# Kernel tuning notes

Measured on AMD Instinct MI355X. Metric: run time of the kernel, lower is better.

The kernel has to match this reference:

```python
import jax, jax.numpy as jnp
import numpy as np
from jax import lax

B, S, V, E, H = 64, 512, 50000, 300, 256


def _run_lstm(x, w_ih, w_hh, b_ih, b_hh, reverse):
    # x: [B,S,D]; w_ih: [4H,D]; w_hh: [4H,H]. PyTorch gate order: i,f,g,o.
    gx = jnp.einsum('bsd,gd->sbg', x, w_ih) + b_ih + b_hh  # [S,B,4H]
    Hh = w_hh.shape[1]

    def step(carry, g):
        h, c = carry
        g = g + h @ w_hh.T
        i, f, gg, o = jnp.split(g, 4, axis=-1)
        c = jax.nn.sigmoid(f) * c + jax.nn.sigmoid(i) * jnp.tanh(gg)
        h = jax.nn.sigmoid(o) * jnp.tanh(c)
        return (h, c), h

    init = (jnp.zeros((x.shape[0], Hh), x.dtype), jnp.zeros((x.shape[0], Hh), x.dtype))
    _, hs = lax.scan(step, init, gx, reverse=reverse)  # outputs aligned to input time order
    return jnp.swapaxes(hs, 0, 1)  # [B,S,H]


def _bilstm(x, wif, whf, bif, bhf, wib, whb, bib, bhb):
    fwd = _run_lstm(x, wif, whf, bif, bhf, False)
    bwd = _run_lstm(x, wib, whb, bib, bhb, True)
    return jnp.concatenate([fwd, bwd], axis=-1)  # [B,S,2H]


def setup_inputs() -> dict:
    key = jax.random.key(0)
    ks = iter(jax.random.split(key, 32))
    k = 1.0 / np.sqrt(H)
    u = lambda shape: jax.random.uniform(next(ks), shape, jnp.float32, -k, k)
    inp = {
        'input_ids': jax.random.randint(next(ks), (B, S), 0, V),
        'labels': jax.random.uniform(next(ks), (B, S), jnp.float32),
        'input_masks': jnp.ones((B, S), jnp.int64),
        'emb': jax.random.normal(next(ks), (V, E), jnp.float32) * 0.1,
    }
    # layer 0 (input E), layer 1 (input 2H); forward and backward directions
    for layer, d_in in ((0, E), (1, 2 * H)):
        for direc in ('f', 'b'):
            inp[f'w_ih_l{layer}{direc}'] = u((4 * H, d_in))
            inp[f'w_hh_l{layer}{direc}'] = u((4 * H, H))
            inp[f'b_ih_l{layer}{direc}'] = u((4 * H,))
            inp[f'b_hh_l{layer}{direc}'] = u((4 * H,))
    inp['w_lin'] = u((H,))
    inp['b_lin'] = u(())
    return inp


def reference(input_ids, labels, input_masks, emb,
              w_ih_l0f, w_hh_l0f, b_ih_l0f, b_hh_l0f,
              w_ih_l0b, w_hh_l0b, b_ih_l0b, b_hh_l0b,
              w_ih_l1f, w_hh_l1f, b_ih_l1f, b_hh_l1f,
              w_ih_l1b, w_hh_l1b, b_ih_l1b, b_hh_l1b,
              w_lin, b_lin):
    x = emb[input_ids]  # one-shot gather, replaces the double python loop: [B,S,E]
    h1 = _bilstm(x, w_ih_l0f, w_hh_l0f, b_ih_l0f, b_hh_l0f,
                 w_ih_l0b, w_hh_l0b, b_ih_l0b, b_hh_l0b)
    h2 = _bilstm(h1, w_ih_l1f, w_hh_l1f, b_ih_l1f, b_hh_l1f,
                 w_ih_l1b, w_hh_l1b, b_ih_l1b, b_hh_l1b)  # [B,S,2H]
    b, s = h2.shape[0], h2.shape[1]
    mean_dir = h2.reshape(b, s, 2, H).mean(axis=2)  # mean over directions
    scores = jax.nn.sigmoid(jnp.einsum('bsh,h->bs', mean_dir, w_lin) + b_lin)
    mask = input_masks.astype(scores.dtype)
    err = (scores - labels) ** 2 * mask
    loss = jnp.mean(jnp.sum(err, axis=1) / jnp.sum(mask, axis=1))
    return scores, loss
```

## Files before the change

### kernel.cpp

```cpp
#include <hip/hip_runtime.h>
#include <hip/hip_bf16.h>
#include <stdint.h>

#define B_  64
#define S_  512
#define E_  300
#define H_  256
#define T_  (B_*S_)
#define G4H 1024

using half8  = __attribute__((ext_vector_type(8))) _Float16;
using half4  = __attribute__((ext_vector_type(4))) _Float16;
using float4v = __attribute__((ext_vector_type(4))) float;

union H2 { _Float16 h[2]; uint32_t u; };

__device__ inline float sigm(float x) { return 1.f / (1.f + __expf(-x)); }
__device__ inline float tanhf_(float x) {
  float cx = fminf(fmaxf(x, -15.f), 15.f);
  float e = __expf(2.f * cx);
  return (e - 1.f) / (e + 1.f);
}

#define BARRIER() asm volatile("s_waitcnt lgkmcnt(0)\n\ts_barrier" ::: "memory")

__device__ inline void ld3_sc0(const uint64_t* p0, const uint64_t* p1,
                               const uint64_t* p2, uint4& a, uint4& b, uint4& c) {
  asm volatile(
      "global_load_dwordx4 %0, %3, off sc0\n\t"
      "global_load_dwordx4 %1, %4, off sc0\n\t"
      "global_load_dwordx4 %2, %5, off sc0\n\t"
      "s_waitcnt vmcnt(0)"
      : "=&v"(a), "=&v"(b), "=&v"(c)
      : "v"(p0), "v"(p1), "v"(p2) : "memory");
}
__device__ inline void st_sc0(uint64_t* p, uint64_t v) {
  asm volatile("global_store_dwordx2 %0, %1, off sc0" :: "v"(p), "v"(v) : "memory");
}
__device__ inline uint4 ldx4_pin(const _Float16* p) {
  uint4 r;
  asm volatile("global_load_dwordx4 %0, %1, off\n\ts_waitcnt vmcnt(0)"
               : "=v"(r) : "v"(p));
  return r;
}
__device__ inline int xcc_id() {
  int x;
  asm volatile("s_getreg_b32 %0, hwreg(HW_REG_XCC_ID, 0, 32)" : "=s"(x));
  return x & 7;
}

__global__ __launch_bounds__(256) void k_prep_wih(const float* __restrict__ wf,
    const float* __restrict__ wb, _Float16* __restrict__ Bt,
    int KIN, int KP, int total)
{
  int idx = blockIdx.x * 256 + threadIdx.x;
  if (idx >= total) return;
  int n = idx / KP, k = idx % KP;
  int dd = n >> 10, nn = n & 1023;
  int row = (nn & 3) * 256 + (nn >> 2);
  const float* src = dd ? wb : wf;
  Bt[idx] = (_Float16)(k < KIN ? src[row * KIN + k] : 0.f);
}

__global__ __launch_bounds__(256) void k_prep_whh(const float* __restrict__ wf,
    const float* __restrict__ wb, _Float16* __restrict__ Wr)
{
  int idx = blockIdx.x * 256 + threadIdx.x;
  int dd = idx >> 18;
  int rem = idx & 262143;
  int n = rem >> 8, k = rem & 255;
  int row = (n & 3) * 256 + (n >> 2);
  Wr[idx] = (_Float16)((dd ? wb : wf)[row * 256 + k]);
}

__global__ void k_prep_bias(const float* __restrict__ bif, const float* __restrict__ bhf,
    const float* __restrict__ bib, const float* __restrict__ bhb, float* __restrict__ bias)
{
  int n = blockIdx.x * 256 + threadIdx.x;
  int dd = n >> 10, nn = n & 1023;
  int row = (nn & 3) * 256 + (nn >> 2);
  bias[n] = dd ? (bib[row] + bhb[row]) : (bif[row] + bhf[row]);
}

__global__ __launch_bounds__(256) void k_gather(const int* __restrict__ ids,
    const float* __restrict__ emb, _Float16* __restrict__ xbf)
{
  int idx = blockIdx.x * 256 + threadIdx.x;
  int tt = idx / 40;
  int ch = idx % 40;
  int b = tt & 63, s = tt >> 6;
  int id = ids[b * S_ + s];
  const float* src = emb + (size_t)id * E_ + ch * 8;
  half8 v;
#pragma unroll
  for (int e = 0; e < 8; ++e) {
    int k = ch * 8 + e;
    v[e] = (_Float16)(k < E_ ? src[e] : 0.f);
  }
  *(half8*)(xbf + (size_t)tt * 320 + ch * 8) = v;
}

template<int K>
__global__ __launch_bounds__(256) void k_gemm(const _Float16* __restrict__ A,
    const _Float16* __restrict__ Bt, const float* __restrict__ bias,
    _Float16* __restrict__ gx)
{
  __shared__ _Float16 sA[128 * 72];
  __shared__ _Float16 sB[128 * 72];
  const int tid = threadIdx.x;
  const int t0 = blockIdx.y * 128;
  const int n0 = blockIdx.x * 128;
  const int lane = tid & 63, wid = tid >> 6;
  const int l15 = lane & 15, q = lane >> 4;
  const int wm = wid & 1, wn = wid >> 1;

  float4v acc[4][4] = {};

  for (int kt = 0; kt < K / 64; ++kt) {
    __syncthreads();
#pragma unroll
    for (int c = 0; c < 4; ++c) {
      int f = tid * 4 + c;
      int row = f >> 3, seg = f & 7;
      *(half8*)&sA[row * 72 + seg * 8] =
          *(const half8*)(A + (size_t)(t0 + row) * K + kt * 64 + seg * 8);
      *(half8*)&sB[row * 72 + seg * 8] =
          *(const half8*)(Bt + (size_t)(n0 + row) * K + kt * 64 + seg * 8);
    }
    __syncthreads();
#pragma unroll
    for (int kk = 0; kk < 2; ++kk) {
      half8 a[4], b[4];
#pragma unroll
      for (int mt = 0; mt < 4; ++mt)
        a[mt] = *(const half8*)&sA[(wm * 64 + mt * 16 + l15) * 72 + kk * 32 + q * 8];
#pragma unroll
      for (int nt = 0; nt < 4; ++nt)
        b[nt] = *(const half8*)&sB[(wn * 64 + nt * 16 + l15) * 72 + kk * 32 + q * 8];
#pragma unroll
      for (int mt = 0; mt < 4; ++mt)
#pragma unroll
        for (int nt = 0; nt < 4; ++nt)
          acc[mt][nt] = __builtin_amdgcn_mfma_f32_16x16x32_f16(a[mt], b[nt], acc[mt][nt], 0, 0, 0);
    }
  }

#pragma unroll
  for (int mt = 0; mt < 4; ++mt) {
#pragma unroll
    for (int nt = 0; nt < 4; ++nt) {
      int token = t0 + wm * 64 + mt * 16 + q * 4;
      int n = n0 + wn * 64 + nt * 16 + l15;
      float bs = bias[n];
      size_t base = (size_t)(n >> 10) * ((size_t)T_ * G4H) + (size_t)token * G4H + (n & 1023);
#pragma unroll
      for (int r = 0; r < 4; ++r)
        gx[base + (size_t)r * G4H] = (_Float16)(acc[mt][nt][r] + bs);
    }
  }
}

template<int LAYER>
__global__ __launch_bounds__(256, 1) void k_rec(const _Float16* __restrict__ gx,
    const _Float16* __restrict__ Wr, uint64_t* __restrict__ hxf,
    uint64_t* __restrict__ hxs, _Float16* __restrict__ h1bf,
    float* __restrict__ pd2, const float* __restrict__ w_lin,
    int* __restrict__ claim)
{
  const int tid = threadIdx.x;
  __shared__ int role_sh;

  if (tid == 0) {
    int xcd = xcc_id();
    int slot = __hip_atomic_fetch_add(claim + xcd, 1, __ATOMIC_RELAXED,
                                      __HIP_MEMORY_SCOPE_AGENT);
    int role = -1;
    if (slot < 4) {
      role = xcd * 4 + slot;
    } else {
      for (int it = 0;; ++it) {
        int s = 0, deficit = -1;
        for (int x = 0; x < 8; ++x) {
          int v = __hip_atomic_load(claim + x, __ATOMIC_RELAXED,
                                    __HIP_MEMORY_SCOPE_AGENT);
          s += (v < 4 ? v : 4);
          if (v < 4) deficit = x;
        }
        if (s == 32) break;
        if (it > 8 && deficit >= 0) {
          int r = __hip_atomic_fetch_add(claim + deficit, 1, __ATOMIC_RELAXED,
                                         __HIP_MEMORY_SCOPE_AGENT);
          if (r < 4) { role = deficit * 4 + r; break; }
        }
        __builtin_amdgcn_s_sleep(64);
      }
    }
    role_sh = role;
  }
  __syncthreads();
  const int role = role_sh;
  if (role < 0) return;

  const int cg = role >> 2, rg = role & 3;
  const int d = cg >> 2, g = cg & 3;
  const int lane = tid & 63, wv = tid >> 6;
  const int l15 = lane & 15, q = lane >> 4;
  const int b0g = g * 16;
  const int n0g = rg * 256;

  __shared__ _Float16 hstage[16 * 288];
  __shared__ float    preS[16 * 260];

  for (int i = tid; i < 16 * 144; i += 256)
    ((uint32_t*)hstage)[i] = 0u;

  uint4 wreg[4][8];
#pragma unroll
  for (int nt = 0; nt < 4; ++nt)
#pragma unroll
    for (int kt = 0; kt < 8; ++kt)
      wreg[nt][kt] = ldx4_pin(Wr +
          (size_t)(d * G4H + n0g + wv * 64 + nt * 16 + l15) * H_ + kt * 32 + q * 8);

  const int bl = tid >> 4;
  const int jl4 = (tid & 15) * 4;
  const int bglob = b0g + bl;
  const int jg = rg * 64 + jl4;
  float wl[4];
#pragma unroll
  for (int cc = 0; cc < 4; ++cc) wl[cc] = w_lin[jg + cc];
  float creg[4] = {0.f, 0.f, 0.f, 0.f};

  uint64_t* fbase = hxf + (size_t)cg * 2 * 2048;
  uint64_t* sbase = hxs + (size_t)cg * 2 * 2048;
  const int off2 = tid * 2;
  const int q2a = (rg + 1) & 3, q2b = (rg + 2) & 3, q2c = (rg + 3) & 3;

  half8 gxa, gxb;
  {
    const int time0 = d ? (S_ - 1) : 0;
    const _Float16* gp = gx + ((size_t)d * T_ + (size_t)time0 * B_ + bglob) * G4H
                           + n0g + (tid & 15) * 16;
    gxa = *(const half8*)(gp);
    gxb = *(const half8*)(gp + 8);
  }

  for (int t = 0; t < S_; ++t) {
    const int time = d ? (S_ - 1 - t) : t;

    if (t > 0) {
      const uint64_t* fs = fbase + (size_t)(t & 1) * 2048;
      const uint64_t* ss = sbase + (size_t)(t & 1) * 2048;
      const uint32_t tt = (uint32_t)t;
      uint32_t dat[6];
      unsigned pend = 0x3fu;
      int round = 0;
      while (pend) {
        uint4 A, Bv, C;
        ld3_sc0(fs + q2a * 512 + off2, fs + q2b * 512 + off2,
                fs + q2c * 512 + off2, A, Bv, C);
        if ((pend & 1u)  && A.y  == tt) { dat[0] = A.x;  pend &= ~1u; }
        if ((pend & 2u)  && A.w  == tt) { dat[1] = A.z;  pend &= ~2u; }
        if ((pend & 4u)  && Bv.y == tt) { dat[2] = Bv.x; pend &= ~4u; }
        if ((pend & 8u)  && Bv.w == tt) { dat[3] = Bv.z; pend &= ~8u; }
        if ((pend & 16u) && C.y  == tt) { dat[4] = C.x;  pend &= ~16u; }
        if ((pend & 32u) && C.w  == tt) { dat[5] = C.z;  pend &= ~32u; }
        if (pend && ((++round & 3) == 0)) {
          const int wq[3] = {q2a, q2b, q2c};
#pragma unroll
          for (int k3 = 0; k3 < 3; ++k3)
#pragma unroll
            for (int j = 0; j < 2; ++j) {
              int w = k3 * 2 + j;
              if (pend & (1u << w)) {
                uint64_t v = __hip_atomic_load(ss + wq[k3] * 512 + off2 + j,
                                               __ATOMIC_RELAXED, __HIP_MEMORY_SCOPE_AGENT);
                if ((uint32_t)(v >> 32) == tt) { dat[w] = (uint32_t)v; pend &= ~(1u << w); }
              }
            }
        }
      }
      const int sb = tid >> 4, jp = (tid & 15) * 2;
      uint2 va; va.x = dat[0]; va.y = dat[1];
      uint2 vb; vb.x = dat[2]; vb.y = dat[3];
      uint2 vc; vc.x = dat[4]; vc.y = dat[5];
      *(uint2*)&((uint32_t*)hstage)[sb * 144 + q2a * 32 + jp] = va;
      *(uint2*)&((uint32_t*)hstage)[sb * 144 + q2b * 32 + jp] = vb;
      *(uint2*)&((uint32_t*)hstage)[sb * 144 + q2c * 32 + jp] = vc;
    }
    BARRIER();

    half8 gxa_n, gxb_n;
    {
      const int tn = (t + 1 < S_) ? t + 1 : t;
      const int timen = d ? (S_ - 1 - tn) : tn;
      const _Float16* gp = gx + ((size_t)d * T_ + (size_t)timen * B_ + bglob) * G4H
                             + n0g + (tid & 15) * 16;
      gxa_n = *(const half8*)(gp);
      gxb_n = *(const half8*)(gp + 8);
    }

    float4v acc[4] = {};
#pragma unroll
    for (int kt = 0; kt < 8; ++kt) {
      half8 a = *(const half8*)&hstage[l15 * 288 + kt * 32 + q * 8];
#pragma unroll
      for (int nt = 0; nt < 4; ++nt)
        acc[nt] = __builtin_amdgcn_mfma_f32_16x16x32_f16(
            a, __builtin_bit_cast(half8, wreg[nt][kt]), acc[nt], 0, 0, 0);
    }
#pragma unroll
    for (int nt = 0; nt < 4; ++nt)
#pragma unroll
      for (int r = 0; r < 4; ++r)
        preS[(q * 4 + r) * 260 + wv * 64 + nt * 16 + l15] = acc[nt][r];
    BARRIER();

    half4 hv4;
    float partial = 0.f;
#pragma unroll
    for (int cc = 0; cc < 4; ++cc) {
      float4v p = *(const float4v*)&preS[bl * 260 + (jl4 + cc) * 4];
      float gxi = (float)(cc < 2 ? gxa[cc * 4 + 0] : gxb[(cc - 2) * 4 + 0]);
      float gxf = (float)(cc < 2 ? gxa[cc * 4 + 1] : gxb[(cc - 2) * 4 + 1]);
      float gxg = (float)(cc < 2 ? gxa[cc * 4 + 2] : gxb[(cc - 2) * 4 + 2]);
      float gxo = (float)(cc < 2 ? gxa[cc * 4 + 3] : gxb[(cc - 2) * 4 + 3]);
      float gi = p[0] + gxi, gf = p[1] + gxf, gg = p[2] + gxg, go = p[3] + gxo;
      float cv = sigm(gf) * creg[cc] + sigm(gi) * tanhf_(gg);
      float hv = sigm(go) * tanhf_(cv);
      creg[cc] = cv;
      hv4[cc] = (_Float16)hv;
      if (LAYER == 1) partial += 0.5f * hv * wl[cc];
    }

    {
      H2 p0; p0.h[0] = hv4[0]; p0.h[1] = hv4[1];
      H2 p1; p1.h[0] = hv4[2]; p1.h[1] = hv4[3];
      uint32_t tg = (uint32_t)(t + 1);
      uint64_t w0 = ((uint64_t)tg << 32) | p0.u;
      uint64_t w1 = ((uint64_t)tg << 32) | p1.u;
      uint64_t* fd = fbase + (size_t)((t + 1) & 1) * 2048 + rg * 512 + off2;
      st_sc0(fd + 0, w0);
      st_sc0(fd + 1, w1);
      uint64_t* sd = sbase + (size_t)((t + 1) & 1) * 2048 + rg * 512 + off2;
      __hip_atomic_store(sd + 0, w0, __ATOMIC_RELAXED, __HIP_MEMORY_SCOPE_AGENT);
      __hip_atomic_store(sd + 1, w1, __ATOMIC_RELAXED, __HIP_MEMORY_SCOPE_AGENT);
    }

    *(half4*)&hstage[bl * 288 + jg] = hv4;

    if (LAYER == 0) {
      *(half4*)(h1bf + ((size_t)time * B_ + bglob) * 512 + d * H_ + jg) = hv4;
    } else {
      partial += __shfl_xor(partial, 1);
      partial += __shfl_xor(partial, 2);
      partial += __shfl_xor(partial, 4);
      partial += __shfl_xor(partial, 8);
      if ((tid & 15) == 0)
        atomicAdd(pd2 + ((size_t)d * B_ + bglob) * S_ + time, partial);
    }

    gxa = gxa_n; gxb = gxb_n;
  }
}

__global__ __launch_bounds__(256) void k_final(const float* __restrict__ pd2,
    const float* __restrict__ labels, const int* __restrict__ masks,
    const float* __restrict__ b_lin, float* __restrict__ out)
{
  int b = blockIdx.x;
  int tid = threadIdx.x;
  float bl = b_lin[0];
  float se = 0.f, sm = 0.f;
  for (int s = tid; s < S_; s += 256) {
    float p = pd2[(size_t)b * S_ + s] + pd2[(size_t)(B_ + b) * S_ + s];
    float sc = sigm(p + bl);
    out[b * S_ + s] = sc;
    float m = (float)masks[b * S_ + s];
    float e = sc - labels[b * S_ + s];
    se += e * e * m;
    sm += m;
  }
  for (int off = 1; off < 64; off <<= 1) {
    se += __shfl_xor(se, off);
    sm += __shfl_xor(sm, off);
  }
  __shared__ float rs[4], rm[4];
  int wid = tid >> 6;
  if ((tid & 63) == 0) { rs[wid] = se; rm[wid] = sm; }
  __syncthreads();
  if (tid == 0) {
    float te = 0.f, tm = 0.f;
    for (int w = 0; w < 4; ++w) { te += rs[w]; tm += rm[w]; }
    atomicAdd(out + T_, (te / tm) * (1.f / 64.f));
  }
}

extern "C" void kernel_launch(void* const* d_in, const int* in_sizes, int n_in,
                              void* d_out, int out_size, void* d_ws, size_t ws_size,
                              hipStream_t stream)
{
  (void)in_sizes; (void)n_in; (void)out_size; (void)ws_size;
  const int*   ids    = (const int*)d_in[0];
  const float* labels = (const float*)d_in[1];
  const int*   masks  = (const int*)d_in[2];
  const float* emb    = (const float*)d_in[3];
  const float* w_ih_0f = (const float*)d_in[4];
  const float* w_hh_0f = (const float*)d_in[5];
  const float* b_ih_0f = (const float*)d_in[6];
  const float* b_hh_0f = (const float*)d_in[7];
  const float* w_ih_0b = (const float*)d_in[8];
  const float* w_hh_0b = (const float*)d_in[9];
  const float* b_ih_0b = (const float*)d_in[10];
  const float* b_hh_0b = (const float*)d_in[11];
  const float* w_ih_1f = (const float*)d_in[12];
  const float* w_hh_1f = (const float*)d_in[13];
  const float* b_ih_1f = (const float*)d_in[14];
  const float* b_hh_1f = (const float*)d_in[15];
  const float* w_ih_1b = (const float*)d_in[16];
  const float* w_hh_1b = (const float*)d_in[17];
  const float* b_ih_1b = (const float*)d_in[18];
  const float* b_hh_1b = (const float*)d_in[19];
  const float* w_lin   = (const float*)d_in[20];
  const float* b_lin   = (const float*)d_in[21];
  float* out = (float*)d_out;

  char* ws = (char*)d_ws;
  size_t off = 0;
  auto alloc = [&](size_t bytes) -> char* {
    char* p = ws + off;
    off += (bytes + 255) & ~(size_t)255;
    return p;
  };
  _Float16* xbf   = (_Float16*)alloc((size_t)T_ * 320 * 2);
  _Float16* h1bf  = (_Float16*)alloc((size_t)T_ * 512 * 2);
  _Float16* gx    = (_Float16*)alloc((size_t)2 * T_ * G4H * 2);
  _Float16* Bt0   = (_Float16*)alloc((size_t)2048 * 320 * 2);
  _Float16* Bt1   = (_Float16*)alloc((size_t)2048 * 512 * 2);
  _Float16* Wr0   = (_Float16*)alloc((size_t)2 * G4H * H_ * 2);
  _Float16* Wr1   = (_Float16*)alloc((size_t)2 * G4H * H_ * 2);
  float*    bias0 = (float*)alloc(2048 * 4);
  float*    bias1 = (float*)alloc(2048 * 4);
  uint64_t* hxf0  = (uint64_t*)alloc((size_t)8 * 2 * 2048 * 8);
  uint64_t* hxs0  = (uint64_t*)alloc((size_t)8 * 2 * 2048 * 8);
  uint64_t* hxf1  = (uint64_t*)alloc((size_t)8 * 2 * 2048 * 8);
  uint64_t* hxs1  = (uint64_t*)alloc((size_t)8 * 2 * 2048 * 8);
  float*    pd2   = (float*)alloc((size_t)2 * B_ * S_ * 4);
  int*      claim0 = (int*)alloc(256);
  int*      claim1 = (int*)alloc(256);

  k_prep_wih<<<(2048 * 320) / 256, 256, 0, stream>>>(w_ih_0f, w_ih_0b, Bt0, 300, 320, 2048 * 320);
  k_prep_wih<<<(2048 * 512) / 256, 256, 0, stream>>>(w_ih_1f, w_ih_1b, Bt1, 512, 512, 2048 * 512);
  k_prep_whh<<<524288 / 256, 256, 0, stream>>>(w_hh_0f, w_hh_0b, Wr0);
  k_prep_whh<<<524288 / 256, 256, 0, stream>>>(w_hh_1f, w_hh_1b, Wr1);
  k_prep_bias<<<8, 256, 0, stream>>>(b_ih_0f, b_hh_0f, b_ih_0b, b_hh_0b, bias0);
  k_prep_bias<<<8, 256, 0, stream>>>(b_ih_1f, b_hh_1f, b_ih_1b, b_hh_1b, bias1);
  k_gather<<<(T_ * 40) / 256, 256, 0, stream>>>(ids, emb, xbf);

  hipMemsetAsync(hxf0, 0, (size_t)8 * 2 * 2048 * 8, stream);
  hipMemsetAsync(hxs0, 0, (size_t)8 * 2 * 2048 * 8, stream);
  hipMemsetAsync(hxf1, 0, (size_t)8 * 2 * 2048 * 8, stream);
  hipMemsetAsync(hxs1, 0, (size_t)8 * 2 * 2048 * 8, stream);
  hipMemsetAsync(pd2, 0, (size_t)2 * B_ * S_ * 4, stream);
  hipMemsetAsync(claim0, 0, 256, stream);
  hipMemsetAsync(claim1, 0, 256, stream);
  hipMemsetAsync((char*)d_out + (size_t)T_ * 4, 0, 4, stream);

  k_gemm<320><<<dim3(16, 256), 256, 0, stream>>>(xbf, Bt0, bias0, gx);
  k_rec<0><<<256, 256, 0, stream>>>(gx, Wr0, hxf0, hxs0, h1bf, pd2, w_lin, claim0);

  k_gemm<512><<<dim3(16, 256), 256, 0, stream>>>(h1bf, Bt1, bias1, gx);
  k_rec<1><<<256, 256, 0, stream>>>(gx, Wr1, hxf1, hxs1, h1bf, pd2, w_lin, claim1);

  k_final<<<64, 256, 0, stream>>>(pd2, labels, masks, b_lin, out);
}
```

Baseline: 3.298 ms.

## Interleave two batch groups per recurrent workgroup to hide cross-block exchange latency

Each recurrent workgroup now owns two 16-row batch groups and alternates between them each timestep, halving the number of participating blocks from 32 to 16. It confines them to four XCDs. While one group computes, the hidden-state exchange loads for the other group are issued early and waited on with a partial vmcnt, so polling latency overlaps with MFMA and gate work. The fallback polling path is replaced by periodic sc0 sc1 reloads from the secondary buffer. The cost is twice the serial work per block and more register and LDS pressure, with fewer CUs in use.

```diff
diff --git a/kernel.cpp b/kernel.cpp
--- a/kernel.cpp
+++ b/kernel.cpp
@@ -15,6 +15,8 @@
 
 union H2 { _Float16 h[2]; uint32_t u; };
 
+template<int N> struct IC { static constexpr int value = N; };
+
 __device__ inline float sigm(float x) { return 1.f / (1.f + __expf(-x)); }
 __device__ inline float tanhf_(float x) {
   float cx = fminf(fmaxf(x, -15.f), 15.f);
@@ -24,6 +26,19 @@
 
 #define BARRIER() asm volatile("s_waitcnt lgkmcnt(0)\n\ts_barrier" ::: "memory")
 
+__device__ inline void ld3_issue(const uint64_t* p0, const uint64_t* p1,
+                                 const uint64_t* p2, uint4& a, uint4& b, uint4& c) {
+  asm volatile(
+      "global_load_dwordx4 %0, %3, off sc0\n\t"
+      "global_load_dwordx4 %1, %4, off sc0\n\t"
+      "global_load_dwordx4 %2, %5, off sc0"
+      : "=&v"(a), "=&v"(b), "=&v"(c)
+      : "v"(p0), "v"(p1), "v"(p2) : "memory");
+}
+__device__ inline void ld3_complete5() {
+  asm volatile("s_waitcnt vmcnt(5)" ::: "memory");
+  __builtin_amdgcn_sched_barrier(0);
+}
 __device__ inline void ld3_sc0(const uint64_t* p0, const uint64_t* p1,
                                const uint64_t* p2, uint4& a, uint4& b, uint4& c) {
   asm volatile(
@@ -34,6 +49,16 @@
       : "=&v"(a), "=&v"(b), "=&v"(c)
       : "v"(p0), "v"(p1), "v"(p2) : "memory");
 }
+__device__ inline void ld3_slow(const uint64_t* p0, const uint64_t* p1,
+                                const uint64_t* p2, uint4& a, uint4& b, uint4& c) {
+  asm volatile(
+      "global_load_dwordx4 %0, %3, off sc0 sc1\n\t"
+      "global_load_dwordx4 %1, %4, off sc0 sc1\n\t"
+      "global_load_dwordx4 %2, %5, off sc0 sc1\n\t"
+      "s_waitcnt vmcnt(0)"
+      : "=&v"(a), "=&v"(b), "=&v"(c)
+      : "v"(p0), "v"(p1), "v"(p2) : "memory");
+}
 __device__ inline void st_sc0(uint64_t* p, uint64_t v) {
   asm volatile("global_store_dwordx2 %0, %1, off sc0" :: "v"(p), "v"(v) : "memory");
 }
@@ -172,21 +197,22 @@
 
   if (tid == 0) {
     int xcd = xcc_id();
-    int slot = __hip_atomic_fetch_add(claim + xcd, 1, __ATOMIC_RELAXED,
-                                      __HIP_MEMORY_SCOPE_AGENT);
     int role = -1;
-    if (slot < 4) {
-      role = xcd * 4 + slot;
-    } else {
+    if (xcd < 4) {
+      int slot = __hip_atomic_fetch_add(claim + xcd, 1, __ATOMIC_RELAXED,
+                                        __HIP_MEMORY_SCOPE_AGENT);
+      if (slot < 4) role = xcd * 4 + slot;
+    }
+    if (role < 0) {
       for (int it = 0;; ++it) {
         int s = 0, deficit = -1;
-        for (int x = 0; x < 8; ++x) {
+        for (int x = 0; x < 4; ++x) {
           int v = __hip_atomic_load(claim + x, __ATOMIC_RELAXED,
                                     __HIP_MEMORY_SCOPE_AGENT);
           s += (v < 4 ? v : 4);
           if (v < 4) deficit = x;
         }
-        if (s == 32) break;
+        if (s == 16) break;
         if (it > 8 && deficit >= 0) {
           int r = __hip_atomic_fetch_add(claim + deficit, 1, __ATOMIC_RELAXED,
                                          __HIP_MEMORY_SCOPE_AGENT);
@@ -201,17 +227,17 @@
   const int role = role_sh;
   if (role < 0) return;
 
-  const int cg = role >> 2, rg = role & 3;
-  const int d = cg >> 2, g = cg & 3;
+  const int set = role >> 2, rg = role & 3;
+  const int d = set >> 1;
+  const int gA = (set & 1) * 2;
   const int lane = tid & 63, wv = tid >> 6;
   const int l15 = lane & 15, q = lane >> 4;
-  const int b0g = g * 16;
   const int n0g = rg * 256;
 
-  __shared__ _Float16 hstage[16 * 288];
+  __shared__ _Float16 hstage[2][16 * 288];
   __shared__ float    preS[16 * 260];
 
-  for (int i = tid; i < 16 * 144; i += 256)
+  for (int i = tid; i < 2 * 16 * 144; i += 256)
     ((uint32_t*)hstage)[i] = 0u;
 
   uint4 wreg[4][8];
@@ -224,86 +250,97 @@
 
   const int bl = tid >> 4;
   const int jl4 = (tid & 15) * 4;
-  const int bglob = b0g + bl;
   const int jg = rg * 64 + jl4;
   float wl[4];
 #pragma unroll
   for (int cc = 0; cc < 4; ++cc) wl[cc] = w_lin[jg + cc];
-  float creg[4] = {0.f, 0.f, 0.f, 0.f};
-
-  uint64_t* fbase = hxf + (size_t)cg * 2 * 2048;
-  uint64_t* sbase = hxs + (size_t)cg * 2 * 2048;
+
+  const int bglob[2] = { gA * 16 + bl, (gA + 1) * 16 + bl };
+  uint64_t* fbuf[2]; uint64_t* sbuf[2];
+#pragma unroll
+  for (int g = 0; g < 2; ++g) {
+    int cg = d * 4 + gA + g;
+    fbuf[g] = hxf + (size_t)cg * 2 * 2048;
+    sbuf[g] = hxs + (size_t)cg * 2 * 2048;
+  }
+  float creg[2][4] = {};
   const int off2 = tid * 2;
   const int q2a = (rg + 1) & 3, q2b = (rg + 2) & 3, q2c = (rg + 3) & 3;
 
-  half8 gxa, gxb;
-  {
+  half8 gxc[2][2];
+#pragma unroll
+  for (int g = 0; g < 2; ++g) {
     const int time0 = d ? (S_ - 1) : 0;
-    const _Float16* gp = gx + ((size_t)d * T_ + (size_t)time0 * B_ + bglob) * G4H
+    const _Float16* gp = gx + ((size_t)d * T_ + (size_t)time0 * B_ + bglob[g]) * G4H
                            + n0g + (tid & 15) * 16;
-    gxa = *(const half8*)(gp);
-    gxb = *(const half8*)(gp + 8);
-  }
-
-  for (int t = 0; t < S_; ++t) {
+    gxc[g][0] = *(const half8*)(gp);
+    gxc[g][1] = *(const half8*)(gp + 8);
+  }
+
+  uint4 sp0 = {0, 0, 0, 0}, sp1 = {0, 0, 0, 0}, sp2 = {0, 0, 0, 0};
+
+  auto phase = [&](auto Gc, int t) {
+    constexpr int G = decltype(Gc)::value;
     const int time = d ? (S_ - 1 - t) : t;
 
     if (t > 0) {
-      const uint64_t* fs = fbase + (size_t)(t & 1) * 2048;
-      const uint64_t* ss = sbase + (size_t)(t & 1) * 2048;
+      const uint64_t* fs = fbuf[G] + (size_t)(t & 1) * 2048;
+      const uint64_t* ss = sbuf[G] + (size_t)(t & 1) * 2048;
       const uint32_t tt = (uint32_t)t;
       uint32_t dat[6];
       unsigned pend = 0x3fu;
+      ld3_complete5();
+      uint4 A = sp0, Bv = sp1, C = sp2;
       int round = 0;
-      while (pend) {
-        uint4 A, Bv, C;
-        ld3_sc0(fs + q2a * 512 + off2, fs + q2b * 512 + off2,
-                fs + q2c * 512 + off2, A, Bv, C);
+      for (;;) {
         if ((pend & 1u)  && A.y  == tt) { dat[0] = A.x;  pend &= ~1u; }
         if ((pend & 2u)  && A.w  == tt) { dat[1] = A.z;  pend &= ~2u; }
         if ((pend & 4u)  && Bv.y == tt) { dat[2] = Bv.x; pend &= ~4u; }
         if ((pend & 8u)  && Bv.w == tt) { dat[3] = Bv.z; pend &= ~8u; }
         if ((pend & 16u) && C.y  == tt) { dat[4] = C.x;  pend &= ~16u; }
         if ((pend & 32u) && C.w  == tt) { dat[5] = C.z;  pend &= ~32u; }
-        if (pend && ((++round & 3) == 0)) {
-          const int wq[3] = {q2a, q2b, q2c};
-#pragma unroll
-          for (int k3 = 0; k3 < 3; ++k3)
-#pragma unroll
-            for (int j = 0; j < 2; ++j) {
-              int w = k3 * 2 + j;
-              if (pend & (1u << w)) {
-                uint64_t v = __hip_atomic_load(ss + wq[k3] * 512 + off2 + j,
-                                               __ATOMIC_RELAXED, __HIP_MEMORY_SCOPE_AGENT);
-                if ((uint32_t)(v >> 32) == tt) { dat[w] = (uint32_t)v; pend &= ~(1u << w); }
-              }
-            }
+        if (!pend) break;
+        if (((++round) & 7) == 0) {
+          ld3_slow(ss + q2a * 512 + off2, ss + q2b * 512 + off2,
+                   ss + q2c * 512 + off2, A, Bv, C);
+        } else {
+          ld3_sc0(fs + q2a * 512 + off2, fs + q2b * 512 + off2,
+                  fs + q2c * 512 + off2, A, Bv, C);
         }
       }
-      const int sb = tid >> 4, jp = (tid & 15) * 2;
+      const int sbr = tid >> 4, jp = (tid & 15) * 2;
       uint2 va; va.x = dat[0]; va.y = dat[1];
       uint2 vb; vb.x = dat[2]; vb.y = dat[3];
       uint2 vc; vc.x = dat[4]; vc.y = dat[5];
-      *(uint2*)&((uint32_t*)hstage)[sb * 144 + q2a * 32 + jp] = va;
-      *(uint2*)&((uint32_t*)hstage)[sb * 144 + q2b * 32 + jp] = vb;
-      *(uint2*)&((uint32_t*)hstage)[sb * 144 + q2c * 32 + jp] = vc;
+      *(uint2*)&((uint32_t*)hstage[G])[sbr * 144 + q2a * 32 + jp] = va;
+      *(uint2*)&((uint32_t*)hstage[G])[sbr * 144 + q2b * 32 + jp] = vb;
+      *(uint2*)&((uint32_t*)hstage[G])[sbr * 144 + q2c * 32 + jp] = vc;
     }
     BARRIER();
 
-    half8 gxa_n, gxb_n;
+    {
+      const int ct = t + G;
+      if (ct >= 1 && ct < S_) {
+        const uint64_t* nfs = fbuf[1 - G] + (size_t)(ct & 1) * 2048;
+        ld3_issue(nfs + q2a * 512 + off2, nfs + q2b * 512 + off2,
+                  nfs + q2c * 512 + off2, sp0, sp1, sp2);
+      }
+    }
+
+    half8 gna, gnb;
     {
       const int tn = (t + 1 < S_) ? t + 1 : t;
       const int timen = d ? (S_ - 1 - tn) : tn;
-      const _Float16* gp = gx + ((size_t)d * T_ + (size_t)timen * B_ + bglob) * G4H
+      const _Float16* gp = gx + ((size_t)d * T_ + (size_t)timen * B_ + bglob[G]) * G4H
                              + n0g + (tid & 15) * 16;
-      gxa_n = *(const half8*)(gp);
-      gxb_n = *(const half8*)(gp + 8);
+      gna = *(const half8*)(gp);
+      gnb = *(const half8*)(gp + 8);
     }
 
     float4v acc[4] = {};
 #pragma unroll
     for (int kt = 0; kt < 8; ++kt) {
-      half8 a = *(const half8*)&hstage[l15 * 288 + kt * 32 + q * 8];
+      half8 a = *(const half8*)&hstage[G][l15 * 288 + kt * 32 + q * 8];
 #pragma unroll
       for (int nt = 0; nt < 4; ++nt)
         acc[nt] = __builtin_amdgcn_mfma_f32_16x16x32_f16(
@@ -321,14 +358,14 @@
 #pragma unroll
     for (int cc = 0; cc < 4; ++cc) {
       float4v p = *(const float4v*)&preS[bl * 260 + (jl4 + cc) * 4];
-      float gxi = (float)(cc < 2 ? gxa[cc * 4 + 0] : gxb[(cc - 2) * 4 + 0]);
-      float gxf = (float)(cc < 2 ? gxa[cc * 4 + 1] : gxb[(cc - 2) * 4 + 1]);
-      float gxg = (float)(cc < 2 ? gxa[cc * 4 + 2] : gxb[(cc - 2) * 4 + 2]);
-      float gxo = (float)(cc < 2 ? gxa[cc * 4 + 3] : gxb[(cc - 2) * 4 + 3]);
+      float gxi = (float)(cc < 2 ? gxc[G][0][cc * 4 + 0] : gxc[G][1][(cc - 2) * 4 + 0]);
+      float gxf = (float)(cc < 2 ? gxc[G][0][cc * 4 + 1] : gxc[G][1][(cc - 2) * 4 + 1]);
+      float gxg = (float)(cc < 2 ? gxc[G][0][cc * 4 + 2] : gxc[G][1][(cc - 2) * 4 + 2]);
+      float gxo = (float)(cc < 2 ? gxc[G][0][cc * 4 + 3] : gxc[G][1][(cc - 2) * 4 + 3]);
       float gi = p[0] + gxi, gf = p[1] + gxf, gg = p[2] + gxg, go = p[3] + gxo;
-      float cv = sigm(gf) * creg[cc] + sigm(gi) * tanhf_(gg);
+      float cv = sigm(gf) * creg[G][cc] + sigm(gi) * tanhf_(gg);
       float hv = sigm(go) * tanhf_(cv);
-      creg[cc] = cv;
+      creg[G][cc] = cv;
       hv4[cc] = (_Float16)hv;
       if (LAYER == 1) partial += 0.5f * hv * wl[cc];
     }
@@ -339,28 +376,33 @@
       uint32_t tg = (uint32_t)(t + 1);
       uint64_t w0 = ((uint64_t)tg << 32) | p0.u;
       uint64_t w1 = ((uint64_t)tg << 32) | p1.u;
-      uint64_t* fd = fbase + (size_t)((t + 1) & 1) * 2048 + rg * 512 + off2;
+      uint64_t* fd = fbuf[G] + (size_t)((t + 1) & 1) * 2048 + rg * 512 + off2;
       st_sc0(fd + 0, w0);
       st_sc0(fd + 1, w1);
-      uint64_t* sd = sbase + (size_t)((t + 1) & 1) * 2048 + rg * 512 + off2;
+      uint64_t* sd = sbuf[G] + (size_t)((t + 1) & 1) * 2048 + rg * 512 + off2;
       __hip_atomic_store(sd + 0, w0, __ATOMIC_RELAXED, __HIP_MEMORY_SCOPE_AGENT);
       __hip_atomic_store(sd + 1, w1, __ATOMIC_RELAXED, __HIP_MEMORY_SCOPE_AGENT);
     }
 
-    *(half4*)&hstage[bl * 288 + jg] = hv4;
+    *(half4*)&hstage[G][bl * 288 + jg] = hv4;
 
     if (LAYER == 0) {
-      *(half4*)(h1bf + ((size_t)time * B_ + bglob) * 512 + d * H_ + jg) = hv4;
+      *(half4*)(h1bf + ((size_t)time * B_ + bglob[G]) * 512 + d * H_ + jg) = hv4;
     } else {
       partial += __shfl_xor(partial, 1);
       partial += __shfl_xor(partial, 2);
       partial += __shfl_xor(partial, 4);
       partial += __shfl_xor(partial, 8);
       if ((tid & 15) == 0)
-        atomicAdd(pd2 + ((size_t)d * B_ + bglob) * S_ + time, partial);
-    }
-
-    gxa = gxa_n; gxb = gxb_n;
+        atomicAdd(pd2 + ((size_t)d * B_ + bglob[G]) * S_ + time, partial);
+    }
+
+    gxc[G][0] = gna; gxc[G][1] = gnb;
+  };
+
+  for (int t = 0; t < S_; ++t) {
+    phase(IC<0>{}, t);
+    phase(IC<1>{}, t);
   }
 }
 
```

Result: slower. 5.331 ms (+61.6%).

## Drop XCD-aware role claiming and use device-scope polling for h exchange

Applied to the files above, without the earlier changes.

Removes the XCD-local role assignment, where 256 blocks raced to claim 32 roles grouped by XCC, and launches exactly 32 blocks with role taken from blockIdx. The two-buffer scheme (fast sc0 path plus atomic fallback) becomes a single buffer polled with sc0 sc1 device-coherent loads and written with agent-scope atomic stores. This removes claiming overhead and the duplicate stores. In exchange, cooperating blocks may sit on different XCDs, so every exchange has to go through device-coherent memory instead of the shared L2.

```diff
diff --git a/kernel.cpp b/kernel.cpp
--- a/kernel.cpp
+++ b/kernel.cpp
@@ -24,29 +24,21 @@
 
 #define BARRIER() asm volatile("s_waitcnt lgkmcnt(0)\n\ts_barrier" ::: "memory")
 
-__device__ inline void ld3_sc0(const uint64_t* p0, const uint64_t* p1,
+__device__ inline void ld3_dev(const uint64_t* p0, const uint64_t* p1,
                                const uint64_t* p2, uint4& a, uint4& b, uint4& c) {
   asm volatile(
-      "global_load_dwordx4 %0, %3, off sc0\n\t"
-      "global_load_dwordx4 %1, %4, off sc0\n\t"
-      "global_load_dwordx4 %2, %5, off sc0\n\t"
+      "global_load_dwordx4 %0, %3, off sc0 sc1\n\t"
+      "global_load_dwordx4 %1, %4, off sc0 sc1\n\t"
+      "global_load_dwordx4 %2, %5, off sc0 sc1\n\t"
       "s_waitcnt vmcnt(0)"
       : "=&v"(a), "=&v"(b), "=&v"(c)
       : "v"(p0), "v"(p1), "v"(p2) : "memory");
-}
-__device__ inline void st_sc0(uint64_t* p, uint64_t v) {
-  asm volatile("global_store_dwordx2 %0, %1, off sc0" :: "v"(p), "v"(v) : "memory");
 }
 __device__ inline uint4 ldx4_pin(const _Float16* p) {
   uint4 r;
   asm volatile("global_load_dwordx4 %0, %1, off\n\ts_waitcnt vmcnt(0)"
                : "=v"(r) : "v"(p));
   return r;
-}
-__device__ inline int xcc_id() {
-  int x;
-  asm volatile("s_getreg_b32 %0, hwreg(HW_REG_XCC_ID, 0, 32)" : "=s"(x));
-  return x & 7;
 }
 
 __global__ __launch_bounds__(256) void k_prep_wih(const float* __restrict__ wf,
@@ -162,45 +154,12 @@
 
 template<int LAYER>
 __global__ __launch_bounds__(256, 1) void k_rec(const _Float16* __restrict__ gx,
-    const _Float16* __restrict__ Wr, uint64_t* __restrict__ hxf,
-    uint64_t* __restrict__ hxs, _Float16* __restrict__ h1bf,
-    float* __restrict__ pd2, const float* __restrict__ w_lin,
-    int* __restrict__ claim)
+    const _Float16* __restrict__ Wr, uint64_t* __restrict__ hx,
+    _Float16* __restrict__ h1bf, float* __restrict__ pd2,
+    const float* __restrict__ w_lin)
 {
   const int tid = threadIdx.x;
-  __shared__ int role_sh;
-
-  if (tid == 0) {
-    int xcd = xcc_id();
-    int slot = __hip_atomic_fetch_add(claim + xcd, 1, __ATOMIC_RELAXED,
-                                      __HIP_MEMORY_SCOPE_AGENT);
-    int role = -1;
-    if (slot < 4) {
-      role = xcd * 4 + slot;
-    } else {
-      for (int it = 0;; ++it) {
-        int s = 0, deficit = -1;
-        for (int x = 0; x < 8; ++x) {
-          int v = __hip_atomic_load(claim + x, __ATOMIC_RELAXED,
-                                    __HIP_MEMORY_SCOPE_AGENT);
-          s += (v < 4 ? v : 4);
-          if (v < 4) deficit = x;
-        }
-        if (s == 32) break;
-        if (it > 8 && deficit >= 0) {
-          int r = __hip_atomic_fetch_add(claim + deficit, 1, __ATOMIC_RELAXED,
-                                         __HIP_MEMORY_SCOPE_AGENT);
-          if (r < 4) { role = deficit * 4 + r; break; }
-        }
-        __builtin_amdgcn_s_sleep(64);
-      }
-    }
-    role_sh = role;
-  }
-  __syncthreads();
-  const int role = role_sh;
-  if (role < 0) return;
-
+  const int role = blockIdx.x;
   const int cg = role >> 2, rg = role & 3;
   const int d = cg >> 2, g = cg & 3;
   const int lane = tid & 63, wv = tid >> 6;
@@ -231,8 +190,7 @@
   for (int cc = 0; cc < 4; ++cc) wl[cc] = w_lin[jg + cc];
   float creg[4] = {0.f, 0.f, 0.f, 0.f};
 
-  uint64_t* fbase = hxf + (size_t)cg * 2 * 2048;
-  uint64_t* sbase = hxs + (size_t)cg * 2 * 2048;
+  uint64_t* base = hx + (size_t)cg * 2 * 2048;
   const int off2 = tid * 2;
   const int q2a = (rg + 1) & 3, q2b = (rg + 2) & 3, q2c = (rg + 3) & 3;
 
@@ -249,36 +207,21 @@
     const int time = d ? (S_ - 1 - t) : t;
 
     if (t > 0) {
-      const uint64_t* fs = fbase + (size_t)(t & 1) * 2048;
-      const uint64_t* ss = sbase + (size_t)(t & 1) * 2048;
+      const uint64_t* ss = base + (size_t)(t & 1) * 2048;
       const uint32_t tt = (uint32_t)t;
       uint32_t dat[6];
       unsigned pend = 0x3fu;
-      int round = 0;
-      while (pend) {
+      for (;;) {
         uint4 A, Bv, C;
-        ld3_sc0(fs + q2a * 512 + off2, fs + q2b * 512 + off2,
-                fs + q2c * 512 + off2, A, Bv, C);
+        ld3_dev(ss + q2a * 512 + off2, ss + q2b * 512 + off2,
+                ss + q2c * 512 + off2, A, Bv, C);
         if ((pend & 1u)  && A.y  == tt) { dat[0] = A.x;  pend &= ~1u; }
         if ((pend & 2u)  && A.w  == tt) { dat[1] = A.z;  pend &= ~2u; }
         if ((pend & 4u)  && Bv.y == tt) { dat[2] = Bv.x; pend &= ~4u; }
         if ((pend & 8u)  && Bv.w == tt) { dat[3] = Bv.z; pend &= ~8u; }
         if ((pend & 16u) && C.y  == tt) { dat[4] = C.x;  pend &= ~16u; }
         if ((pend & 32u) && C.w  == tt) { dat[5] = C.z;  pend &= ~32u; }
-        if (pend && ((++round & 3) == 0)) {
-          const int wq[3] = {q2a, q2b, q2c};
-#pragma unroll
-          for (int k3 = 0; k3 < 3; ++k3)
-#pragma unroll
-            for (int j = 0; j < 2; ++j) {
-              int w = k3 * 2 + j;
-              if (pend & (1u << w)) {
-                uint64_t v = __hip_atomic_load(ss + wq[k3] * 512 + off2 + j,
-                                               __ATOMIC_RELAXED, __HIP_MEMORY_SCOPE_AGENT);
-                if ((uint32_t)(v >> 32) == tt) { dat[w] = (uint32_t)v; pend &= ~(1u << w); }
-              }
-            }
-        }
+        if (!pend) break;
       }
       const int sb = tid >> 4, jp = (tid & 15) * 2;
       uint2 va; va.x = dat[0]; va.y = dat[1];
@@ -339,10 +282,7 @@
       uint32_t tg = (uint32_t)(t + 1);
       uint64_t w0 = ((uint64_t)tg << 32) | p0.u;
       uint64_t w1 = ((uint64_t)tg << 32) | p1.u;
-      uint64_t* fd = fbase + (size_t)((t + 1) & 1) * 2048 + rg * 512 + off2;
-      st_sc0(fd + 0, w0);
-      st_sc0(fd + 1, w1);
-      uint64_t* sd = sbase + (size_t)((t + 1) & 1) * 2048 + rg * 512 + off2;
+      uint64_t* sd = base + (size_t)((t + 1) & 1) * 2048 + rg * 512 + off2;
       __hip_atomic_store(sd + 0, w0, __ATOMIC_RELAXED, __HIP_MEMORY_SCOPE_AGENT);
       __hip_atomic_store(sd + 1, w1, __ATOMIC_RELAXED, __HIP_MEMORY_SCOPE_AGENT);
     }
@@ -441,13 +381,9 @@
   _Float16* Wr1   = (_Float16*)alloc((size_t)2 * G4H * H_ * 2);
   float*    bias0 = (float*)alloc(2048 * 4);
   float*    bias1 = (float*)alloc(2048 * 4);
-  uint64_t* hxf0  = (uint64_t*)alloc((size_t)8 * 2 * 2048 * 8);
-  uint64_t* hxs0  = (uint64_t*)alloc((size_t)8 * 2 * 2048 * 8);
-  uint64_t* hxf1  = (uint64_t*)alloc((size_t)8 * 2 * 2048 * 8);
-  uint64_t* hxs1  = (uint64_t*)alloc((size_t)8 * 2 * 2048 * 8);
+  uint64_t* hx0   = (uint64_t*)alloc((size_t)8 * 2 * 2048 * 8);
+  uint64_t* hx1   = (uint64_t*)alloc((size_t)8 * 2 * 2048 * 8);
   float*    pd2   = (float*)alloc((size_t)2 * B_ * S_ * 4);
-  int*      claim0 = (int*)alloc(256);
-  int*      claim1 = (int*)alloc(256);
 
   k_prep_wih<<<(2048 * 320) / 256, 256, 0, stream>>>(w_ih_0f, w_ih_0b, Bt0, 300, 320, 2048 * 320);
   k_prep_wih<<<(2048 * 512) / 256, 256, 0, stream>>>(w_ih_1f, w_ih_1b, Bt1, 512, 512, 2048 * 512);
@@ -457,20 +393,16 @@
   k_prep_bias<<<8, 256, 0, stream>>>(b_ih_1f, b_hh_1f, b_ih_1b, b_hh_1b, bias1);
   k_gather<<<(T_ * 40) / 256, 256, 0, stream>>>(ids, emb, xbf);
 
-  hipMemsetAsync(hxf0, 0, (size_t)8 * 2 * 2048 * 8, stream);
-  hipMemsetAsync(hxs0, 0, (size_t)8 * 2 * 2048 * 8, stream);
-  hipMemsetAsync(hxf1, 0, (size_t)8 * 2 * 2048 * 8, stream);
-  hipMemsetAsync(hxs1, 0, (size_t)8 * 2 * 2048 * 8, stream);
+  hipMemsetAsync(hx0, 0, (size_t)8 * 2 * 2048 * 8, stream);
+  hipMemsetAsync(hx1, 0, (size_t)8 * 2 * 2048 * 8, stream);
   hipMemsetAsync(pd2, 0, (size_t)2 * B_ * S_ * 4, stream);
-  hipMemsetAsync(claim0, 0, 256, stream);
-  hipMemsetAsync(claim1, 0, 256, stream);
   hipMemsetAsync((char*)d_out + (size_t)T_ * 4, 0, 4, stream);
 
   k_gemm<320><<<dim3(16, 256), 256, 0, stream>>>(xbf, Bt0, bias0, gx);
-  k_rec<0><<<256, 256, 0, stream>>>(gx, Wr0, hxf0, hxs0, h1bf, pd2, w_lin, claim0);
+  k_rec<0><<<32, 256, 0, stream>>>(gx, Wr0, hx0, h1bf, pd2, w_lin);
 
   k_gemm<512><<<dim3(16, 256), 256, 0, stream>>>(h1bf, Bt1, bias1, gx);
-  k_rec<1><<<256, 256, 0, stream>>>(gx, Wr1, hxf1, hxs1, h1bf, pd2, w_lin, claim1);
+  k_rec<1><<<32, 256, 0, stream>>>(gx, Wr1, hx1, h1bf, pd2, w_lin);
 
   k_final<<<64, 256, 0, stream>>>(pd2, labels, masks, b_lin, out);
 }
```

Measured after the change: 2.846 ms. 13.7% less time.
